# Kernel optimization log

Hardware: AMD Instinct MI355X
Metric: run time of the kernel (lower is better)

## Reference

```python
import jax, jax.numpy as jnp
import numpy as np

# Flax nn.LSTMCell math: gates i,f,g,o; input dense has no bias, hidden dense has bias.
# We fuse the four gate projections into single [D,4H] / [H,4H] matrices in order (i,f,g,o).

def _lstm_layer(x, Wx, Wh, b):
    # x: [B,T,D], Wx: [D,4H], Wh: [H,4H], b: [4H]
    B = x.shape[0]
    H = Wh.shape[0]
    # Precompute input projections for the whole sequence (one big GEMM).
    xW = jnp.einsum('btd,dg->btg', x, Wx) + b  # [B,T,4H]

    def step(carry, xw_t):
        c, h = carry
        z = xw_t + h @ Wh  # [B,4H]
        i, f, g, o = jnp.split(z, 4, axis=-1)
        i = jax.nn.sigmoid(i)
        f = jax.nn.sigmoid(f)
        g = jnp.tanh(g)
        o = jax.nn.sigmoid(o)
        c = f * c + i * g
        h = o * jnp.tanh(c)
        return (c, h), h

    init = (jnp.zeros((B, H), x.dtype), jnp.zeros((B, H), x.dtype))
    _, ys = jax.lax.scan(step, init, jnp.swapaxes(xW, 0, 1))  # scan over T
    return jnp.swapaxes(ys, 0, 1)  # [B,T,H]


def setup_inputs() -> dict:
    key = jax.random.key(0)
    ks = jax.random.split(key, 7)
    B, T, D, H = 64, 512, 512, 1024
    s = lambda fan_in: 1.0 / np.sqrt(fan_in)
    x = jax.random.normal(ks[0], (B, T, D), dtype=jnp.float32)
    Wx0 = jax.random.normal(ks[1], (D, 4 * H), dtype=jnp.float32) * s(D)
    Wh0 = jax.random.normal(ks[2], (H, 4 * H), dtype=jnp.float32) * s(H)
    b0 = jnp.zeros((4 * H,), dtype=jnp.float32)
    Wx1 = jax.random.normal(ks[3], (H, 4 * H), dtype=jnp.float32) * s(H)
    Wh1 = jax.random.normal(ks[4], (H, 4 * H), dtype=jnp.float32) * s(H)
    b1 = jnp.zeros((4 * H,), dtype=jnp.float32)
    return {"x": x, "Wx0": Wx0, "Wh0": Wh0, "b0": b0, "Wx1": Wx1, "Wh1": Wh1, "b1": b1}


def reference(x, Wx0, Wh0, b0, Wx1, Wh1, b1):
    h1 = _lstm_layer(x, Wx0, Wh0, b0)
    h2 = _lstm_layer(h1, Wx1, Wh1, b1)
    return h2
```

## Files before the change

### kernel.cpp

```cpp
#include <hip/hip_runtime.h>

typedef __attribute__((ext_vector_type(8))) short short8;
typedef __attribute__((ext_vector_type(4))) float f32x4;

#define WS_XB     0ull
#define WS_W0T    33554432ull
#define WS_W1T    46137344ull
#define WS_RING0  62914560ull
#define WS_RING1  67108864ull
#define WS_BAR    71303168ull
#define SLOT_ELEMS 65536
#define SLOT_BYTES 131072

#define BAR_ARR(g)  ((g) * 16)
#define BAR_ROOT    256
#define BAR_REL(g)  (272 + (g) * 16)

__device__ __forceinline__ unsigned short f2bf(float f) {
  unsigned u = __float_as_uint(f);
  u += 0x7FFFu + ((u >> 16) & 1u);
  return (unsigned short)(u >> 16);
}

__device__ __forceinline__ float sigm(float x) { return 1.0f / (1.0f + __expf(-x)); }

__global__ void sentinel_kernel(float* out) { out[0] = 1.0e6f; }

__global__ void convert_x_kernel(const float* __restrict__ x, unsigned short* __restrict__ xb) {
  int i = blockIdx.x * 256 + threadIdx.x;
  const float4 v = ((const float4*)x)[i];
  unsigned long long pack = (unsigned long long)f2bf(v.x)
                          | ((unsigned long long)f2bf(v.y) << 16)
                          | ((unsigned long long)f2bf(v.z) << 32)
                          | ((unsigned long long)f2bf(v.w) << 48);
  ((unsigned long long*)xb)[i] = pack;
}

__global__ void transpose_weights_kernel(const float* __restrict__ wx, const float* __restrict__ wh,
                                         unsigned short* __restrict__ dst, int Kx, int Ktot) {
  __shared__ float tile[32][33];
  const int k0 = blockIdx.x * 32, n0 = blockIdx.y * 32;
  const int tx = threadIdx.x, ty = threadIdx.y;
#pragma unroll
  for (int i = 0; i < 4; ++i) {
    int k = k0 + ty + i * 8;
    tile[ty + i * 8][tx] = (k < Kx) ? wx[(size_t)k * 4096 + n0 + tx]
                                    : wh[(size_t)(k - Kx) * 4096 + n0 + tx];
  }
  __syncthreads();
#pragma unroll
  for (int i = 0; i < 4; ++i) {
    int n = n0 + ty + i * 8;
    int r = (n & 1023) * 4 + (n >> 10);
    dst[(size_t)r * Ktot + k0 + tx] = f2bf(tile[tx][ty + i * 8]);
  }
}

template<int N1, int NBLK>
__device__ __forceinline__ void lstm_step_mfma(int a0b, int a1b,
    const unsigned short* __restrict__ r1p, const unsigned short* __restrict__ r2p,
    f32x4& acc0, f32x4& acc1)
{
  extern __shared__ unsigned short lds[];
  short8 buf[NBLK][8];

#pragma unroll
  for (int bp = 0; bp < NBLK; ++bp) {
    const unsigned short* p = (bp < N1) ? (r1p + bp * 256) : (r2p + (bp - N1) * 256);
#pragma unroll
    for (int j = 0; j < 8; ++j) buf[bp][j] = *(const short8*)(p + j * 32);
  }
  __builtin_amdgcn_sched_barrier(0);

#pragma unroll
  for (int bp = 0; bp < NBLK; ++bp) {
#pragma unroll
    for (int j = 0; j < 8; ++j)
      asm volatile("" :: "v"(buf[bp][j]));
    __builtin_amdgcn_sched_barrier(0);
#pragma unroll
    for (int j = 0; j < 8; ++j) {
      const int ko = bp * 256 + j * 32;
      short8 a0 = *(const short8*)&lds[a0b + ko];
      short8 a1 = *(const short8*)&lds[a1b + ko];
      acc0 = __builtin_amdgcn_mfma_f32_16x16x32_bf16(a0, buf[bp][j], acc0, 0, 0, 0);
      acc1 = __builtin_amdgcn_mfma_f32_16x16x32_bf16(a1, buf[bp][j], acc1, 0, 0, 0);
    }
  }
}

__global__ void __launch_bounds__(256, 1) lstm_persistent(
    const unsigned short* __restrict__ xb,
    const unsigned short* __restrict__ w0t,
    const unsigned short* __restrict__ w1t,
    const float* __restrict__ b0v, const float* __restrict__ b1v,
    unsigned short* __restrict__ ring0, unsigned short* __restrict__ ring1,
    unsigned* __restrict__ bar,
    float* __restrict__ out)
{
  extern __shared__ unsigned short lds[];

  const int wg    = blockIdx.x;
  const int group = wg >> 7;
  const int wgl   = wg & 127;
  const int hu0   = wgl * 8;
  const int tid   = threadIdx.x;
  const int lane  = tid & 63;
  const int wid   = tid >> 6;
  const int c16   = lane & 15;
  const int row4  = lane >> 4;
  const int bb    = wid * 16 + c16;

  const int K    = group ? 2048 : 1536;
  const int KPAD = group ? 2056 : 1544;

  {
    const unsigned short* wsrc = (group ? w1t : w0t) + (size_t)(wgl * 32) * K;
    const int kv = K >> 3;
    for (int c = tid; c < 32 * kv; c += 256) {
      int r = c / kv, q = c - r * kv;
      int srcr = 8 * ((r & 15) >> 2) + 4 * (r >> 4) + (r & 3);
      *(short8*)&lds[r * KPAD + q * 8] = *(const short8*)&wsrc[(size_t)srcr * K + q * 8];
    }
  }
  __syncthreads();

  const float* bsrc = group ? b1v : b0v;
  float bias0[4], bias1[4];
#pragma unroll
  for (int j = 0; j < 4; ++j) {
    bias0[j] = bsrc[j * 1024 + hu0 + 2 * row4];
    bias1[j] = bsrc[j * 1024 + hu0 + 2 * row4 + 1];
  }

  const int a0b = c16 * KPAD + 8 * row4;
  const int a1b = a0b + 16 * KPAD;

  const int lofs = (bb << 10) + 8 * row4;
  const unsigned short* x_cur = xb + ((size_t)bb << 18) + 8 * row4;
  unsigned* rwb = (unsigned*)(group ? ring1 : ring0) + (((bb << 10) + hu0) >> 1) + row4;
  float* out_base = out + ((size_t)bb << 19) + hu0 + 2 * row4;

  const int mygrp = wg >> 4;
  unsigned* grpc  = bar + BAR_ARR(mygrp);
  unsigned* rootc = bar + BAR_ROOT;
  unsigned* relc  = bar + BAR_REL(mygrp);

  float cst0 = 0.0f, cst1 = 0.0f;

  for (int s = 0; s <= 512; ++s) {
    const bool active = group ? (s >= 1) : (s < 512);
    if (active) {
      const int t = group ? (s - 1) : s;

      f32x4 acc0 = { bias0[0], bias0[1], bias0[2], bias0[3] };
      f32x4 acc1 = { bias1[0], bias1[1], bias1[2], bias1[3] };

      const unsigned short* h0rd = ring0 + ((s - 1) & 31) * SLOT_ELEMS + lofs;
      if (group == 0) {
        lstm_step_mfma<2, 6>(a0b, a1b, x_cur, h0rd, acc0, acc1);
        x_cur += 512;
      } else {
        const unsigned short* h1rd = ring1 + ((s - 2) & 31) * SLOT_ELEMS + lofs;
        lstm_step_mfma<4, 8>(a0b, a1b, h0rd, h1rd, acc0, acc1);
      }

      float hv0, hv1;
      {
        float iv = sigm(acc0[0]), fv = sigm(acc0[1]);
        float gv = tanhf(acc0[2]), ov = sigm(acc0[3]);
        cst0 = fv * cst0 + iv * gv;
        hv0 = ov * tanhf(cst0);
      }
      {
        float iv = sigm(acc1[0]), fv = sigm(acc1[1]);
        float gv = tanhf(acc1[2]), ov = sigm(acc1[3]);
        cst1 = fv * cst1 + iv * gv;
        hv1 = ov * tanhf(cst1);
      }
      unsigned hp = (unsigned)f2bf(hv0) | ((unsigned)f2bf(hv1) << 16);
      (void)__hip_atomic_exchange(rwb + (t & 31) * (SLOT_ELEMS / 2), hp,
                                  __ATOMIC_RELAXED, __HIP_MEMORY_SCOPE_AGENT);
      if (group) {
        float2 o2; o2.x = hv0; o2.y = hv1;
        *(float2*)(out_base + ((size_t)t << 10)) = o2;
      }
    }

    __syncthreads();
    if (tid == 0) {
      unsigned old = __hip_atomic_fetch_add(grpc, 1u, __ATOMIC_RELAXED, __HIP_MEMORY_SCOPE_AGENT);
      if (old == (unsigned)(16 * s + 15)) {
        unsigned old2 = __hip_atomic_fetch_add(rootc, 1u, __ATOMIC_RELAXED, __HIP_MEMORY_SCOPE_AGENT);
        if (old2 == (unsigned)(16 * s + 15)) {
#pragma unroll
          for (int g2 = 0; g2 < 16; ++g2)
            (void)__hip_atomic_exchange(bar + BAR_REL(g2), (unsigned)(s + 1),
                                        __ATOMIC_RELAXED, __HIP_MEMORY_SCOPE_AGENT);
        }
      }
      while (__hip_atomic_load(relc, __ATOMIC_RELAXED, __HIP_MEMORY_SCOPE_AGENT) < (unsigned)(s + 1))
        __builtin_amdgcn_s_sleep(1);
    }
    __syncthreads();
  }
}

extern "C" void kernel_launch(void* const* d_in, const int* in_sizes, int n_in,
                              void* d_out, int out_size, void* d_ws, size_t ws_size,
                              hipStream_t stream) {
  const float* x   = (const float*)d_in[0];
  const float* Wx0 = (const float*)d_in[1];
  const float* Wh0 = (const float*)d_in[2];
  const float* b0  = (const float*)d_in[3];
  const float* Wx1 = (const float*)d_in[4];
  const float* Wh1 = (const float*)d_in[5];
  const float* b1  = (const float*)d_in[6];
  float* outp = (float*)d_out;

  char* ws = (char*)d_ws;
  unsigned short* xbp   = (unsigned short*)(ws + WS_XB);
  unsigned short* w0tp  = (unsigned short*)(ws + WS_W0T);
  unsigned short* w1tp  = (unsigned short*)(ws + WS_W1T);
  unsigned short* ring0 = (unsigned short*)(ws + WS_RING0);
  unsigned short* ring1 = (unsigned short*)(ws + WS_RING1);
  unsigned*       barp  = (unsigned*)(ws + WS_BAR);

  sentinel_kernel<<<dim3(1), dim3(1), 0, stream>>>(outp);
  convert_x_kernel<<<dim3(16384), dim3(256), 0, stream>>>(x, xbp);
  transpose_weights_kernel<<<dim3(48, 128), dim3(32, 8), 0, stream>>>(Wx0, Wh0, w0tp, 512, 1536);
  transpose_weights_kernel<<<dim3(64, 128), dim3(32, 8), 0, stream>>>(Wx1, Wh1, w1tp, 1024, 2048);
  hipMemsetAsync(ring0 + 31 * SLOT_ELEMS, 0, SLOT_BYTES, stream);
  hipMemsetAsync(ring1 + 31 * SLOT_ELEMS, 0, SLOT_BYTES, stream);
  hipMemsetAsync(barp, 0, 4096, stream);

  void* kargs[] = { (void*)&xbp, (void*)&w0tp, (void*)&w1tp, (void*)&b0, (void*)&b1,
                    (void*)&ring0, (void*)&ring1, (void*)&barp, (void*)&outp };
  hipError_t e = hipLaunchCooperativeKernel((void*)lstm_persistent, dim3(256), dim3(256),
                                            kargs, 32 * 2056 * 2 , stream);
  if (e != hipSuccess) {
    lstm_persistent<<<dim3(256), dim3(256), 32 * 2056 * 2, stream>>>(
        xbp, w0tp, w1tp, b0, b1, ring0, ring1, barp, outp);
  }
}
```

Measured before the change: 5.863 ms.

## Prefetch next-step inputs after layer-0 completion, before full grid barrier release

```diff
diff --git a/kernel.cpp b/kernel.cpp
--- a/kernel.cpp
+++ b/kernel.cpp
@@ -15,6 +15,7 @@
 #define BAR_ARR(g)  ((g) * 16)
 #define BAR_ROOT    256
 #define BAR_REL(g)  (272 + (g) * 16)
+#define BAR_L0DONE  544
 
 __device__ __forceinline__ unsigned short f2bf(float f) {
   unsigned u = __float_as_uint(f);
@@ -53,39 +54,6 @@
     int n = n0 + ty + i * 8;
     int r = (n & 1023) * 4 + (n >> 10);
     dst[(size_t)r * Ktot + k0 + tx] = f2bf(tile[tx][ty + i * 8]);
-  }
-}
-
-template<int N1, int NBLK>
-__device__ __forceinline__ void lstm_step_mfma(int a0b, int a1b,
-    const unsigned short* __restrict__ r1p, const unsigned short* __restrict__ r2p,
-    f32x4& acc0, f32x4& acc1)
-{
-  extern __shared__ unsigned short lds[];
-  short8 buf[NBLK][8];
-
-#pragma unroll
-  for (int bp = 0; bp < NBLK; ++bp) {
-    const unsigned short* p = (bp < N1) ? (r1p + bp * 256) : (r2p + (bp - N1) * 256);
-#pragma unroll
-    for (int j = 0; j < 8; ++j) buf[bp][j] = *(const short8*)(p + j * 32);
-  }
-  __builtin_amdgcn_sched_barrier(0);
-
-#pragma unroll
-  for (int bp = 0; bp < NBLK; ++bp) {
-#pragma unroll
-    for (int j = 0; j < 8; ++j)
-      asm volatile("" :: "v"(buf[bp][j]));
-    __builtin_amdgcn_sched_barrier(0);
-#pragma unroll
-    for (int j = 0; j < 8; ++j) {
-      const int ko = bp * 256 + j * 32;
-      short8 a0 = *(const short8*)&lds[a0b + ko];
-      short8 a1 = *(const short8*)&lds[a1b + ko];
-      acc0 = __builtin_amdgcn_mfma_f32_16x16x32_bf16(a0, buf[bp][j], acc0, 0, 0, 0);
-      acc1 = __builtin_amdgcn_mfma_f32_16x16x32_bf16(a1, buf[bp][j], acc1, 0, 0, 0);
-    }
   }
 }
 
@@ -137,7 +105,7 @@
   const int a1b = a0b + 16 * KPAD;
 
   const int lofs = (bb << 10) + 8 * row4;
-  const unsigned short* x_cur = xb + ((size_t)bb << 18) + 8 * row4;
+  const unsigned short* xbase = xb + ((size_t)bb << 18) + 8 * row4;
   unsigned* rwb = (unsigned*)(group ? ring1 : ring0) + (((bb << 10) + hu0) >> 1) + row4;
   float* out_base = out + ((size_t)bb << 19) + hu0 + 2 * row4;
 
@@ -145,8 +113,22 @@
   unsigned* grpc  = bar + BAR_ARR(mygrp);
   unsigned* rootc = bar + BAR_ROOT;
   unsigned* relc  = bar + BAR_REL(mygrp);
+  unsigned* l0d   = bar + BAR_L0DONE;
 
   float cst0 = 0.0f, cst1 = 0.0f;
+
+  short8 pf0[8], pf1[8], pf2[8], pf3[8];
+
+  auto ld8 = [&](short8* d, const unsigned short* p) {
+#pragma unroll
+    for (int j = 0; j < 8; ++j) d[j] = *(const short8*)(p + j * 32);
+  };
+
+  if (group == 0) {
+    ld8(pf0, xbase); ld8(pf1, xbase + 256);
+    const unsigned short* h0p = ring0 + 31 * SLOT_ELEMS + lofs;
+    ld8(pf2, h0p); ld8(pf3, h0p + 256);
+  }
 
   for (int s = 0; s <= 512; ++s) {
     const bool active = group ? (s >= 1) : (s < 512);
@@ -156,13 +138,29 @@
       f32x4 acc0 = { bias0[0], bias0[1], bias0[2], bias0[3] };
       f32x4 acc1 = { bias1[0], bias1[1], bias1[2], bias1[3] };
 
+      auto mfma8 = [&](const short8* b, int bp) {
+#pragma unroll
+        for (int j = 0; j < 8; ++j) {
+          const int ko = bp * 256 + j * 32;
+          short8 a0 = *(const short8*)&lds[a0b + ko];
+          short8 a1 = *(const short8*)&lds[a1b + ko];
+          acc0 = __builtin_amdgcn_mfma_f32_16x16x32_bf16(a0, b[j], acc0, 0, 0, 0);
+          acc1 = __builtin_amdgcn_mfma_f32_16x16x32_bf16(a1, b[j], acc1, 0, 0, 0);
+        }
+      };
+
       const unsigned short* h0rd = ring0 + ((s - 1) & 31) * SLOT_ELEMS + lofs;
       if (group == 0) {
-        lstm_step_mfma<2, 6>(a0b, a1b, x_cur, h0rd, acc0, acc1);
-        x_cur += 512;
+        short8 f0[8], f1[8];
+        ld8(f0, h0rd + 512); ld8(f1, h0rd + 768);
+        mfma8(pf0, 0); mfma8(pf1, 1); mfma8(pf2, 2); mfma8(pf3, 3);
+        mfma8(f0, 4);  mfma8(f1, 5);
       } else {
         const unsigned short* h1rd = ring1 + ((s - 2) & 31) * SLOT_ELEMS + lofs;
-        lstm_step_mfma<4, 8>(a0b, a1b, h0rd, h1rd, acc0, acc1);
+        short8 f0[8], f1[8], f2[8], f3[8];
+        ld8(f0, h1rd); ld8(f1, h1rd + 256); ld8(f2, h1rd + 512); ld8(f3, h1rd + 768);
+        mfma8(pf0, 0); mfma8(pf1, 1); mfma8(pf2, 2); mfma8(pf3, 3);
+        mfma8(f0, 4);  mfma8(f1, 5);  mfma8(f2, 6);  mfma8(f3, 7);
       }
 
       float hv0, hv1;
@@ -191,6 +189,8 @@
     if (tid == 0) {
       unsigned old = __hip_atomic_fetch_add(grpc, 1u, __ATOMIC_RELAXED, __HIP_MEMORY_SCOPE_AGENT);
       if (old == (unsigned)(16 * s + 15)) {
+        if (group == 0)
+          __hip_atomic_fetch_add(l0d, 1u, __ATOMIC_RELAXED, __HIP_MEMORY_SCOPE_AGENT);
         unsigned old2 = __hip_atomic_fetch_add(rootc, 1u, __ATOMIC_RELAXED, __HIP_MEMORY_SCOPE_AGENT);
         if (old2 == (unsigned)(16 * s + 15)) {
 #pragma unroll
@@ -199,6 +199,28 @@
                                         __ATOMIC_RELAXED, __HIP_MEMORY_SCOPE_AGENT);
         }
       }
+      if (s < 512) {
+        while (__hip_atomic_load(l0d, __ATOMIC_RELAXED, __HIP_MEMORY_SCOPE_AGENT) < 8u * (unsigned)(s + 1))
+          __builtin_amdgcn_s_sleep(1);
+      }
+    }
+    __syncthreads();
+
+    if (s < 512) {
+      const unsigned short* h0n = ring0 + (s & 31) * SLOT_ELEMS + lofs;
+      if (group == 0) {
+        if (s + 1 < 512) {
+          const unsigned short* xn = xbase + (size_t)(s + 1) * 512;
+          ld8(pf0, xn); ld8(pf1, xn + 256);
+          ld8(pf2, h0n); ld8(pf3, h0n + 256);
+        }
+      } else {
+        ld8(pf0, h0n); ld8(pf1, h0n + 256); ld8(pf2, h0n + 512); ld8(pf3, h0n + 768);
+      }
+    }
+    __builtin_amdgcn_sched_barrier(0);
+
+    if (tid == 0) {
       while (__hip_atomic_load(relc, __ATOMIC_RELAXED, __HIP_MEMORY_SCOPE_AGENT) < (unsigned)(s + 1))
         __builtin_amdgcn_s_sleep(1);
     }
```

Measured after the change: 5.633 ms. 3.9% less time.
